# Performance work log

Hardware: AMD Instinct MI355X
Metric: run time of the kernel (lower is better)

The kernel has to match this reference:

```python
import jax, jax.numpy as jnp
import numpy as np

# ---- static configuration (matches init_kwargs) ----
D_MODEL = 512
N_HEAD = 16
HEAD_DIM = D_MODEL // N_HEAD
SCALE = HEAD_DIM ** -0.5
SIZE = (64, 64)
WINDOW = (8, 8)
SHIFT = (4, 4)
WS = WINDOW[0] * WINDOW[1]          # tokens per window = 64
NW = (SIZE[0] // WINDOW[0]) * (SIZE[1] // WINDOW[1])  # windows per sample = 64


def _rel_pos_index(window):
    w0, w1 = window
    coords = np.stack(np.meshgrid(np.arange(w0), np.arange(w1), indexing='ij')).reshape(2, -1)
    rel = (coords[:, :, None] - coords[:, None, :]).transpose(1, 2, 0)  # [ws, ws, 2]
    rel[:, :, 0] += w0 - 1
    rel[:, :, 1] += w1 - 1
    rel[:, :, 0] *= 2 * w1 - 1
    return rel.sum(-1)  # [ws, ws] in [0, (2w0-1)(2w1-1))


def _shift_mask(size, window, shift):
    # Swin-style attention mask for shifted windows: 1.0 where tokens belong
    # to different cyclic-shift regions, else 0.0. Shape [nw, ws, ws].
    H, W = size
    w0, w1 = window
    s0, s1 = shift
    img = np.zeros((H, W))
    cnt = 0
    h_slices = (slice(0, -w0), slice(-w0, -s0), slice(-s0, None)) if s0 > 0 else (slice(None),)
    w_slices = (slice(0, -w1), slice(-w1, -s1), slice(-s1, None)) if s1 > 0 else (slice(None),)
    for hs in h_slices:
        for ws_ in w_slices:
            img[hs, ws_] = cnt
            cnt += 1
    win = img.reshape(H // w0, w0, W // w1, w1).transpose(0, 2, 1, 3).reshape(-1, w0 * w1)
    return (win[:, None, :] != win[:, :, None]).astype(np.float32)


REL_IDX = jnp.asarray(_rel_pos_index(WINDOW))              # [ws, ws] int
MASK = jnp.asarray(-100.0 * _shift_mask(SIZE, WINDOW, SHIFT))  # [nw, ws, ws]


def setup_inputs() -> dict:
    key = jax.random.key(0)
    k1, k2, k3, k4 = jax.random.split(key, 4)
    x = jax.random.normal(k1, (8, SIZE[0], SIZE[1], D_MODEL), dtype=jnp.float32)
    qkv_w = jax.random.normal(k2, (3 * D_MODEL, D_MODEL), dtype=jnp.float32) * (D_MODEL ** -0.5)
    qkv_b = jax.random.normal(k3, (3 * D_MODEL,), dtype=jnp.float32) * 0.02
    bias_table = jax.random.normal(k4, ((2 * WINDOW[0] - 1) * (2 * WINDOW[1] - 1), N_HEAD), dtype=jnp.float32) * 0.02
    return {"x": x, "qkv_w": qkv_w, "qkv_b": qkv_b, "bias_table": bias_table}


def reference(x, qkv_w, qkv_b, bias_table):
    n, H, W, c = x.shape
    w0, w1 = WINDOW
    # --- window partition: [n, H, W, c] -> [n*nw, ws, c] ---
    part = x.reshape(n, H // w0, w0, W // w1, w1, c)
    part = part.transpose(0, 1, 3, 2, 4, 5).reshape(n * NW, WS, c)
    # --- qkv projection ---
    qkv = (part @ qkv_w.T + qkv_b).reshape(n * NW, WS, 3, N_HEAD, HEAD_DIM)
    q, k, v = qkv[:, :, 0] * SCALE, qkv[:, :, 1], qkv[:, :, 2]
    # --- scores + relative bias + shift mask + softmax ---
    attn = jnp.einsum('wihd,wjhd->whij', q, k)  # [n*nw, nh, ws, ws]
    bias = bias_table[REL_IDX].transpose(2, 0, 1)  # [nh, ws, ws]
    attn = attn.reshape(n, NW, N_HEAD, WS, WS) + bias[None, None] + MASK[None, :, None]
    attn = jax.nn.softmax(attn, axis=-1).reshape(n * NW, N_HEAD, WS, WS)
    # --- AV + unpartition ---
    out = jnp.einsum('whij,wjhd->wihd', attn, v).reshape(n * NW, WS, c)
    out = out.reshape(n, H // w0, W // w1, w0, w1, c)
    return out.transpose(0, 1, 3, 2, 4, 5).reshape(n, H, W, c)
```

## Files before the change

### kernel.cpp

```cpp
#include <hip/hip_runtime.h>
#include <stdint.h>

typedef unsigned short u16;
typedef __attribute__((ext_vector_type(4))) float floatx4;
typedef __attribute__((ext_vector_type(8))) short bf16x8;

#define MTOK   32768
#define KDIM   512
#define NQKV   1536
#define NWIN   512
#define N_HEAD 16
#define SECSZ  (512 * 16 * 2048)
#define QK_SCALE 0.17677669529663687f

__device__ __forceinline__ u16 f2bf(float f) {
  union { float f; unsigned u; } v; v.f = f;
  unsigned r = v.u + 0x7fffu + ((v.u >> 16) & 1u);
  return (u16)(r >> 16);
}

__device__ __forceinline__ void load_lds16(const void* g, void* l) {
  __builtin_amdgcn_global_load_lds((const __attribute__((address_space(1))) void*)g,
                                   (__attribute__((address_space(3))) void*)l,
                                   16, 0, 0);
}

__global__ __launch_bounds__(256) void convert_w_tbl(const float* __restrict__ wsrc,
                                                     const float* __restrict__ btab,
                                                     u16* __restrict__ Wb,
                                                     float* __restrict__ tbl) {
  int b = blockIdx.x;
  if (b < 768) {
    int e = (b * 256 + threadIdx.x) * 4;
    const float4 v = *(const float4*)(wsrc + e);
    ushort4 o;
    o.x = f2bf(v.x); o.y = f2bf(v.y); o.z = f2bf(v.z); o.w = f2bf(v.w);
    *(ushort4*)(Wb + e) = o;
  } else {
    int q = b - 768;
    int cls = q >> 4, hh = q & 15;
    int ey = cls >> 1, ex = cls & 1;
    float* To = tbl + (q << 12);
#pragma unroll
    for (int e = 0; e < 16; ++e) {
      int idx = e * 256 + threadIdx.x;
      int i = idx >> 6, j = idx & 63;
      int ty = i >> 3, tx = i & 7, sy = j >> 3, sx = j & 7;
      int ry = ey ? (ty < 4 ? 1 : 2) : 0;
      int rx = ex ? (tx < 4 ? 1 : 2) : 0;
      int qy = ey ? (sy < 4 ? 1 : 2) : 0;
      int qx = ex ? (sx < 4 ? 1 : 2) : 0;
      float v = btab[((ty - sy + 7) * 15 + (tx - sx + 7)) * 16 + hh];
      if (ry * 3 + rx != qy * 3 + qx) v -= 100.0f;
      To[idx] = v;
    }
  }
}

__global__ __launch_bounds__(256, 4) void gemm_qkv(const float* __restrict__ x,
                                                   const u16* __restrict__ Wb,
                                                   const float* __restrict__ bias,
                                                   u16* __restrict__ QKV) {
  __shared__ __attribute__((aligned(16))) char smem[18432];
  u16* Ct = (u16*)smem;

  int b = blockIdx.x;
  int xcd = b & 7, slot = b >> 3;
  int mtile = (slot / 12) * 8 + xcd;
  int ntile = slot % 12;

  int tid = threadIdx.x;
  int wv = tid >> 6, lane = tid & 63;
  int il = lane & 15, ch = lane >> 4;
  int wm = (wv & 1) * 64, wn = (wv >> 1) * 64;

  floatx4 acc[4][4];
  floatx4 zacc = {0.f, 0.f, 0.f, 0.f};
#pragma unroll
  for (int m = 0; m < 4; ++m)
#pragma unroll
    for (int n = 0; n < 4; ++n) acc[m][n] = zacc;

  int row0 = tid >> 2;
  int ch4 = (tid & 3) ^ (row0 & 3);
  int T0 = mtile * 128 + row0;
  int T1 = T0 + 64;
  int w0 = T0 >> 6, t0 = T0 & 63;
  int w1 = T1 >> 6, t1 = T1 & 63;
  const float* px0 = x + ((((w0 >> 6) * 64 + ((w0 >> 3) & 7) * 8 + (t0 >> 3)) * 64
                           + (w0 & 7) * 8 + (t0 & 7)) * 512 + ch4 * 8);
  const float* px1 = x + ((((w1 >> 6) * 64 + ((w1 >> 3) & 7) * 8 + (t1 >> 3)) * 64
                           + (w1 & 7) * 8 + (t1 & 7)) * 512 + ch4 * 8);

  const u16* Bbase = Wb + (ntile * 128 + row0) * KDIM + ch4 * 8;
  char* lBb = smem + 8192;
  char* lB0 = lBb + wv * 1024;
  char* lB1 = lBb + 4096 + wv * 1024;
  char* lAb = smem;

  int sw = il & 3;
  for (int kb = 0; kb < KDIM; kb += 32) {
    __syncthreads();
    load_lds16(Bbase + kb, lB0);
    load_lds16(Bbase + kb + 64 * KDIM, lB1);
    float4 a00 = *(const float4*)(px0 + kb);
    float4 a01 = *(const float4*)(px0 + kb + 4);
    float4 a10 = *(const float4*)(px1 + kb);
    float4 a11 = *(const float4*)(px1 + kb + 4);
    bf16x8 p0, p1;
    p0[0] = (short)f2bf(a00.x); p0[1] = (short)f2bf(a00.y);
    p0[2] = (short)f2bf(a00.z); p0[3] = (short)f2bf(a00.w);
    p0[4] = (short)f2bf(a01.x); p0[5] = (short)f2bf(a01.y);
    p0[6] = (short)f2bf(a01.z); p0[7] = (short)f2bf(a01.w);
    p1[0] = (short)f2bf(a10.x); p1[1] = (short)f2bf(a10.y);
    p1[2] = (short)f2bf(a10.z); p1[3] = (short)f2bf(a10.w);
    p1[4] = (short)f2bf(a11.x); p1[5] = (short)f2bf(a11.y);
    p1[6] = (short)f2bf(a11.z); p1[7] = (short)f2bf(a11.w);
    *(bf16x8*)(lAb + tid * 16) = p0;
    *(bf16x8*)(lAb + 4096 + tid * 16) = p1;
    __syncthreads();

    bf16x8 af[4], bfr[4];
#pragma unroll
    for (int mt = 0; mt < 4; ++mt)
      af[mt] = *(const bf16x8*)(lAb + (wm + mt * 16 + il) * 64 + (ch ^ sw) * 16);
#pragma unroll
    for (int nt = 0; nt < 4; ++nt)
      bfr[nt] = *(const bf16x8*)(lBb + (wn + nt * 16 + il) * 64 + (ch ^ sw) * 16);
#pragma unroll
    for (int mt = 0; mt < 4; ++mt)
#pragma unroll
      for (int nt = 0; nt < 4; ++nt)
        acc[mt][nt] = __builtin_amdgcn_mfma_f32_16x16x32_bf16(af[mt], bfr[nt], acc[mt][nt], 0, 0, 0);
  }

  __syncthreads();

  int sec = ntile >> 2;
  int h0 = (ntile & 3) * 4;
  int gw0 = mtile * 2;
  u16* dst = QKV + (size_t)sec * SECSZ;
  float sc = (sec == 0) ? QK_SCALE : 1.0f;

  for (int p = 0; p < 2; ++p) {
    if ((wv & 1) == p) {
      if (sec < 2) {
#pragma unroll
        for (int nt = 0; nt < 4; ++nt) {
          float bv = bias[ntile * 128 + wn + nt * 16 + il];
          int cl = wn + nt * 16 + il;
#pragma unroll
          for (int mt = 0; mt < 4; ++mt) {
            int lr = mt * 16 + ch * 4;
#pragma unroll
            for (int r = 0; r < 4; ++r)
              Ct[(lr + r) * 136 + cl] = f2bf((acc[mt][nt][r] + bv) * sc);
          }
        }
      } else {
#pragma unroll
        for (int nt = 0; nt < 4; ++nt) {
          float bv = bias[ntile * 128 + wn + nt * 16 + il];
          int cl = wn + nt * 16 + il;
#pragma unroll
          for (int mt = 0; mt < 4; ++mt) {
            int lr = mt * 16 + ch * 4;
            ushort4 pk;
            pk.x = f2bf(acc[mt][nt][0] + bv);
            pk.y = f2bf(acc[mt][nt][1] + bv);
            pk.z = f2bf(acc[mt][nt][2] + bv);
            pk.w = f2bf(acc[mt][nt][3] + bv);
            *(ushort4*)(Ct + cl * 72 + lr) = pk;
          }
        }
      }
    }
    __syncthreads();

    if (sec < 2) {
      int tl = tid >> 2, dc = tid & 3;
#pragma unroll
      for (int hl = 0; hl < 4; ++hl) {
        uint4 v = *(const uint4*)(smem + tl * 272 + hl * 64 + dc * 16);
        *(uint4*)(dst + ((gw0 + p) * 16 + h0 + hl) * 2048 + tl * 32 + dc * 8) = v;
      }
    } else {
      int c0 = tid >> 3, tq = tid & 7;
#pragma unroll
      for (int hl = 0; hl < 4; ++hl) {
        uint4 v = *(const uint4*)(smem + (hl * 32 + c0) * 144 + tq * 16);
        *(uint4*)(dst + ((gw0 + p) * 16 + h0 + hl) * 2048 + c0 * 64 + tq * 8) = v;
      }
    }
    __syncthreads();
  }
}

__global__ __launch_bounds__(256) void attn(const u16* __restrict__ QKV,
                                            const float* __restrict__ tbl,
                                            float* __restrict__ out) {
  __shared__ __attribute__((aligned(16))) u16 Pl[64 * 88];

  int bid = blockIdx.x;
  int w = bid >> 4, h = bid & 15;
  int tid = threadIdx.x;

  int lane = tid & 63, wv = tid >> 6;
  int il = lane & 15, ch = lane >> 4;
  const u16* Qb = QKV + (w * 16 + h) * 2048;
  const u16* Kb = Qb + SECSZ;
  const u16* Vt = Qb + 2 * (size_t)SECSZ;

  bf16x8 aq = *(const bf16x8*)(Qb + (wv * 16 + il) * 32 + ch * 8);
  floatx4 zacc = {0.f, 0.f, 0.f, 0.f};
  floatx4 s[4];
#pragma unroll
  for (int jt = 0; jt < 4; ++jt) {
    bf16x8 bk = *(const bf16x8*)(Kb + (jt * 16 + il) * 32 + ch * 8);
    s[jt] = __builtin_amdgcn_mfma_f32_16x16x32_bf16(aq, bk, zacc, 0, 0, 0);
  }

  int winidx = w & 63;
  int wy = winidx >> 3, wx = winidx & 7;
  int cls = ((wy == 7) ? 2 : 0) | ((wx == 7) ? 1 : 0);
  const float* T = tbl + (((cls << 4) | h) << 12);

  float val[4][4];
#pragma unroll
  for (int r = 0; r < 4; ++r) {
    int i = wv * 16 + ch * 4 + r;
#pragma unroll
    for (int jt = 0; jt < 4; ++jt)
      val[r][jt] = s[jt][r] + T[i * 64 + jt * 16 + il];
  }

#pragma unroll
  for (int r = 0; r < 4; ++r) {
    float m = fmaxf(fmaxf(val[r][0], val[r][1]), fmaxf(val[r][2], val[r][3]));
    m = fmaxf(m, __shfl_xor(m, 1, 64));
    m = fmaxf(m, __shfl_xor(m, 2, 64));
    m = fmaxf(m, __shfl_xor(m, 4, 64));
    m = fmaxf(m, __shfl_xor(m, 8, 64));
    float sum = 0.f;
#pragma unroll
    for (int jt = 0; jt < 4; ++jt) { val[r][jt] = __expf(val[r][jt] - m); sum += val[r][jt]; }
    sum += __shfl_xor(sum, 1, 64);
    sum += __shfl_xor(sum, 2, 64);
    sum += __shfl_xor(sum, 4, 64);
    sum += __shfl_xor(sum, 8, 64);
    float inv = 1.0f / sum;
    int i = wv * 16 + ch * 4 + r;
#pragma unroll
    for (int jt = 0; jt < 4; ++jt)
      Pl[i * 88 + jt * 16 + il] = f2bf(val[r][jt] * inv);
  }

  __syncthreads();

  floatx4 o0 = zacc, o1 = zacc;
#pragma unroll
  for (int kk = 0; kk < 2; ++kk) {
    bf16x8 ap  = *(const bf16x8*)((const u16*)Pl + (wv * 16 + il) * 88 + kk * 32 + ch * 8);
    bf16x8 bv0 = *(const bf16x8*)(Vt + il * 64 + kk * 32 + ch * 8);
    bf16x8 bv1 = *(const bf16x8*)(Vt + (16 + il) * 64 + kk * 32 + ch * 8);
    o0 = __builtin_amdgcn_mfma_f32_16x16x32_bf16(ap, bv0, o0, 0, 0, 0);
    o1 = __builtin_amdgcn_mfma_f32_16x16x32_bf16(ap, bv1, o1, 0, 0, 0);
  }

  int img = w >> 6;
#pragma unroll
  for (int r = 0; r < 4; ++r) {
    int i = wv * 16 + ch * 4 + r;
    int ty = i >> 3, tx = i & 7;
    int y = wy * 8 + ty, xp = wx * 8 + tx;
    float* op = out + ((img * 64 + y) * 64 + xp) * 512 + h * 32;
    op[il] = o0[r];
    op[16 + il] = o1[r];
  }
}

extern "C" void kernel_launch(void* const* d_in, const int* in_sizes, int n_in,
                              void* d_out, int out_size, void* d_ws, size_t ws_size,
                              hipStream_t stream) {
  const float* x      = (const float*)d_in[0];
  const float* qkv_w  = (const float*)d_in[1];
  const float* qkv_b  = (const float*)d_in[2];
  const float* btab   = (const float*)d_in[3];
  float* out = (float*)d_out;

  char* ws = (char*)d_ws;
  u16* Wb    = (u16*)ws;
  u16* QKV   = (u16*)(ws + (size_t)NQKV * KDIM * 2);
  float* tbl = (float*)(ws + (size_t)NQKV * KDIM * 2 + 3 * (size_t)SECSZ * 2);

  convert_w_tbl<<<dim3(832), dim3(256), 0, stream>>>(qkv_w, btab, Wb, tbl);
  gemm_qkv<<<dim3(3072), dim3(256), 0, stream>>>(x, Wb, qkv_b, QKV);
  attn<<<dim3(NWIN * N_HEAD), dim3(256), 0, stream>>>(QKV, tbl, out);
}
```

Baseline: 234.8 us.

## Register-prefetch next x tile in QKV GEMM and hoist V loads in attention

In the QKV projection GEMM, the K loop is unrolled by two and the fp32 x loads for the next 32-wide K slice are issued into registers before the MFMA work on the current slice, so global latency overlaps compute. In the attention kernel, the V fragment loads move ahead of the softmax. The block-wide barrier before the P·V step becomes an LDS wait plus a sched barrier, which is valid because each wave only reads back its own rows of P. This costs extra registers, which may lower occupancy.

New measurement: 241.0 us. 2.7% more time.

```diff
diff --git a/kernel.cpp b/kernel.cpp
--- a/kernel.cpp
+++ b/kernel.cpp
@@ -93,46 +93,76 @@
                            + (w1 & 7) * 8 + (t1 & 7)) * 512 + ch4 * 8);
 
   const u16* Bbase = Wb + (ntile * 128 + row0) * KDIM + ch4 * 8;
+  char* lAb = smem;
   char* lBb = smem + 8192;
   char* lB0 = lBb + wv * 1024;
   char* lB1 = lBb + 4096 + wv * 1024;
-  char* lAb = smem;
+
+#define STAGE_A(q0, q1, q2, q3)                                        \
+  {                                                                    \
+    bf16x8 p0, p1;                                                     \
+    p0[0] = (short)f2bf(q0.x); p0[1] = (short)f2bf(q0.y);              \
+    p0[2] = (short)f2bf(q0.z); p0[3] = (short)f2bf(q0.w);              \
+    p0[4] = (short)f2bf(q1.x); p0[5] = (short)f2bf(q1.y);              \
+    p0[6] = (short)f2bf(q1.z); p0[7] = (short)f2bf(q1.w);              \
+    p1[0] = (short)f2bf(q2.x); p1[1] = (short)f2bf(q2.y);              \
+    p1[2] = (short)f2bf(q2.z); p1[3] = (short)f2bf(q2.w);              \
+    p1[4] = (short)f2bf(q3.x); p1[5] = (short)f2bf(q3.y);              \
+    p1[6] = (short)f2bf(q3.z); p1[7] = (short)f2bf(q3.w);              \
+    *(bf16x8*)(lAb + tid * 16) = p0;                                   \
+    *(bf16x8*)(lAb + 4096 + tid * 16) = p1;                            \
+  }
+
+#define COMPUTE()                                                      \
+  {                                                                    \
+    bf16x8 af[4], bfr[4];                                              \
+    _Pragma("unroll")                                                  \
+    for (int mt = 0; mt < 4; ++mt)                                     \
+      af[mt] = *(const bf16x8*)(lAb + (wm + mt * 16 + il) * 64 + (ch ^ sw) * 16); \
+    _Pragma("unroll")                                                  \
+    for (int nt = 0; nt < 4; ++nt)                                     \
+      bfr[nt] = *(const bf16x8*)(lBb + (wn + nt * 16 + il) * 64 + (ch ^ sw) * 16); \
+    _Pragma("unroll")                                                  \
+    for (int mt = 0; mt < 4; ++mt)                                     \
+      _Pragma("unroll")                                                \
+      for (int nt = 0; nt < 4; ++nt)                                   \
+        acc[mt][nt] = __builtin_amdgcn_mfma_f32_16x16x32_bf16(af[mt], bfr[nt], acc[mt][nt], 0, 0, 0); \
+  }
 
   int sw = il & 3;
-  for (int kb = 0; kb < KDIM; kb += 32) {
+  float4 xA0 = *(const float4*)(px0);
+  float4 xA1 = *(const float4*)(px0 + 4);
+  float4 xA2 = *(const float4*)(px1);
+  float4 xA3 = *(const float4*)(px1 + 4);
+  float4 xB0, xB1, xB2, xB3;
+
+  for (int kb = 0; kb < KDIM; kb += 64) {
     __syncthreads();
     load_lds16(Bbase + kb, lB0);
     load_lds16(Bbase + kb + 64 * KDIM, lB1);
-    float4 a00 = *(const float4*)(px0 + kb);
-    float4 a01 = *(const float4*)(px0 + kb + 4);
-    float4 a10 = *(const float4*)(px1 + kb);
-    float4 a11 = *(const float4*)(px1 + kb + 4);
-    bf16x8 p0, p1;
-    p0[0] = (short)f2bf(a00.x); p0[1] = (short)f2bf(a00.y);
-    p0[2] = (short)f2bf(a00.z); p0[3] = (short)f2bf(a00.w);
-    p0[4] = (short)f2bf(a01.x); p0[5] = (short)f2bf(a01.y);
-    p0[6] = (short)f2bf(a01.z); p0[7] = (short)f2bf(a01.w);
-    p1[0] = (short)f2bf(a10.x); p1[1] = (short)f2bf(a10.y);
-    p1[2] = (short)f2bf(a10.z); p1[3] = (short)f2bf(a10.w);
-    p1[4] = (short)f2bf(a11.x); p1[5] = (short)f2bf(a11.y);
-    p1[6] = (short)f2bf(a11.z); p1[7] = (short)f2bf(a11.w);
-    *(bf16x8*)(lAb + tid * 16) = p0;
-    *(bf16x8*)(lAb + 4096 + tid * 16) = p1;
-    __syncthreads();
-
-    bf16x8 af[4], bfr[4];
-#pragma unroll
-    for (int mt = 0; mt < 4; ++mt)
-      af[mt] = *(const bf16x8*)(lAb + (wm + mt * 16 + il) * 64 + (ch ^ sw) * 16);
-#pragma unroll
-    for (int nt = 0; nt < 4; ++nt)
-      bfr[nt] = *(const bf16x8*)(lBb + (wn + nt * 16 + il) * 64 + (ch ^ sw) * 16);
-#pragma unroll
-    for (int mt = 0; mt < 4; ++mt)
-#pragma unroll
-      for (int nt = 0; nt < 4; ++nt)
-        acc[mt][nt] = __builtin_amdgcn_mfma_f32_16x16x32_bf16(af[mt], bfr[nt], acc[mt][nt], 0, 0, 0);
-  }
+    STAGE_A(xA0, xA1, xA2, xA3);
+    __syncthreads();
+    xB0 = *(const float4*)(px0 + kb + 32);
+    xB1 = *(const float4*)(px0 + kb + 36);
+    xB2 = *(const float4*)(px1 + kb + 32);
+    xB3 = *(const float4*)(px1 + kb + 36);
+    COMPUTE();
+
+    __syncthreads();
+    load_lds16(Bbase + kb + 32, lB0);
+    load_lds16(Bbase + kb + 32 + 64 * KDIM, lB1);
+    STAGE_A(xB0, xB1, xB2, xB3);
+    __syncthreads();
+    if (kb + 64 < KDIM) {
+      xA0 = *(const float4*)(px0 + kb + 64);
+      xA1 = *(const float4*)(px0 + kb + 68);
+      xA2 = *(const float4*)(px1 + kb + 64);
+      xA3 = *(const float4*)(px1 + kb + 68);
+    }
+    COMPUTE();
+  }
+#undef STAGE_A
+#undef COMPUTE
 
   __syncthreads();
 
@@ -220,6 +250,13 @@
     s[jt] = __builtin_amdgcn_mfma_f32_16x16x32_bf16(aq, bk, zacc, 0, 0, 0);
   }
 
+  bf16x8 bv0[2], bv1[2];
+#pragma unroll
+  for (int kk = 0; kk < 2; ++kk) {
+    bv0[kk] = *(const bf16x8*)(Vt + il * 64 + kk * 32 + ch * 8);
+    bv1[kk] = *(const bf16x8*)(Vt + (16 + il) * 64 + kk * 32 + ch * 8);
+  }
+
   int winidx = w & 63;
   int wy = winidx >> 3, wx = winidx & 7;
   int cls = ((wy == 7) ? 2 : 0) | ((wx == 7) ? 1 : 0);
@@ -255,16 +292,15 @@
       Pl[i * 88 + jt * 16 + il] = f2bf(val[r][jt] * inv);
   }
 
-  __syncthreads();
+  asm volatile("s_waitcnt lgkmcnt(0)" ::: "memory");
+  __builtin_amdgcn_sched_barrier(0);
 
   floatx4 o0 = zacc, o1 = zacc;
 #pragma unroll
   for (int kk = 0; kk < 2; ++kk) {
-    bf16x8 ap  = *(const bf16x8*)((const u16*)Pl + (wv * 16 + il) * 88 + kk * 32 + ch * 8);
-    bf16x8 bv0 = *(const bf16x8*)(Vt + il * 64 + kk * 32 + ch * 8);
-    bf16x8 bv1 = *(const bf16x8*)(Vt + (16 + il) * 64 + kk * 32 + ch * 8);
-    o0 = __builtin_amdgcn_mfma_f32_16x16x32_bf16(ap, bv0, o0, 0, 0, 0);
-    o1 = __builtin_amdgcn_mfma_f32_16x16x32_bf16(ap, bv1, o1, 0, 0, 0);
+    bf16x8 ap = *(const bf16x8*)((const u16*)Pl + (wv * 16 + il) * 88 + kk * 32 + ch * 8);
+    o0 = __builtin_amdgcn_mfma_f32_16x16x32_bf16(ap, bv0[kk], o0, 0, 0, 0);
+    o1 = __builtin_amdgcn_mfma_f32_16x16x32_bf16(ap, bv1[kk], o1, 0, 0, 0);
   }
 
   int img = w >> 6;
```
